# Kernel optimization log

Hardware: AMD Instinct MI355X
Metric: run time of the kernel (lower is better)

The kernel has to match this reference:

```python
import jax, jax.numpy as jnp
import numpy as np

N = 10000      # nodes
E = 100000     # edges
H = 256        # hidden_dim
HEADS = 4
HD = H // HEADS
G = 8          # graphs in batch
SPG = N // G   # nodes per graph (equal-size graphs -> to_dense_batch is a reshape)
IN = 16        # in_dim
PE = 5         # pe_dims
ED = 8         # edge_dim
OUT = 4        # out_dim
L = 5          # num_layers


def setup_inputs() -> dict:
    key = jax.random.key(0)
    ks = iter(jax.random.split(key, 64))
    rn = lambda shape, s=0.05: jax.random.normal(next(ks), shape, jnp.float32) * s
    inp = {}
    inp['x'] = jax.random.normal(next(ks), (N, IN), jnp.float32)
    inp['pe'] = jax.random.normal(next(ks), (N, PE), jnp.float32)
    inp['edge_attr'] = jax.random.normal(next(ks), (E, ED), jnp.float32)
    inp['edge_index'] = jax.random.randint(next(ks), (2, E), 0, N, jnp.int32)
    inp['batch'] = (jnp.arange(N) // SPG).astype(jnp.int32)
    # node encoders (3 node types), stacked
    inp['enc_w1'] = rn((3, IN + PE, H)); inp['enc_b1'] = rn((3, H))
    inp['enc_w2'] = rn((3, H, H));       inp['enc_b2'] = rn((3, H))
    # edge encoder
    inp['ee_w1'] = rn((ED, H)); inp['ee_b1'] = rn((H,))
    inp['ee_w2'] = rn((H, H));  inp['ee_b2'] = rn((H,))
    # per-layer edge / node update MLPs, stacked over layers
    inp['eu_w1'] = rn((L, 3 * H, H)); inp['eu_b1'] = rn((L, H))
    inp['eu_w2'] = rn((L, H, H));     inp['eu_b2'] = rn((L, H))
    inp['nu_w1'] = rn((L, 2 * H, H)); inp['nu_b1'] = rn((L, H))
    inp['nu_w2'] = rn((L, H, H));     inp['nu_b2'] = rn((L, H))
    # MultiheadAttention (combined in-proj + out-proj)
    inp['qkv_w'] = rn((H, 3 * H)); inp['qkv_b'] = rn((3 * H,))
    inp['out_w'] = rn((H, H));     inp['out_b'] = rn((H,))
    # fusion MLP
    inp['fu_w1'] = rn((H, H)); inp['fu_b1'] = rn((H,))
    inp['fu_w2'] = rn((H, H)); inp['fu_b2'] = rn((H,))
    # decoders (3 node types)
    inp['dec_w1'] = rn((3, H, H));   inp['dec_b1'] = rn((3, H))
    inp['dec_w2'] = rn((3, H, OUT)); inp['dec_b2'] = rn((3, OUT))
    return inp


def _mlp(z, w1, b1, w2, b2):
    return jnp.maximum(z @ w1 + b1, 0.0) @ w2 + b2


def reference(x, pe, edge_attr, edge_index, batch,
              enc_w1, enc_b1, enc_w2, enc_b2,
              ee_w1, ee_b1, ee_w2, ee_b2,
              eu_w1, eu_b1, eu_w2, eu_b2,
              nu_w1, nu_b1, nu_w2, nu_b2,
              qkv_w, qkv_b, out_w, out_b,
              fu_w1, fu_b1, fu_w2, fu_b2,
              dec_w1, dec_b1, dec_w2, dec_b2):
    n = x.shape[0]
    node_types = (jnp.clip(jnp.round(x[:, 2] * 3.0), 1.0, 3.0).astype(jnp.int32) - 1)
    rng_n = jnp.arange(n)

    # node encoding: run all 3 type-MLPs, select per node (masked dispatch in torch)
    inp = jnp.concatenate([x, pe], axis=-1)                       # [N, IN+PE]
    hid = jnp.maximum(jnp.einsum('ni,tih->tnh', inp, enc_w1) + enc_b1[:, None, :], 0.0)
    h_all = jnp.einsum('tnh,tho->tno', hid, enc_w2) + enc_b2[:, None, :]  # [3,N,H]
    h_nodes = h_all[node_types, rng_n]                            # [N, H]

    h_edges = _mlp(edge_attr, ee_w1, ee_b1, ee_w2, ee_b2)         # [E, H]

    src, dst = edge_index[0], edge_index[1]
    for l in range(L):
        e_in = jnp.concatenate([h_nodes[src], h_nodes[dst], h_edges], axis=-1)  # [E,3H]
        h_edges = h_edges + _mlp(e_in, eu_w1[l], eu_b1[l], eu_w2[l], eu_b2[l])
        m_node = jax.ops.segment_sum(h_edges, dst, num_segments=n)              # index_add_
        n_in = jnp.concatenate([h_nodes, m_node], axis=-1)                      # [N,2H]
        h_nodes = h_nodes + _mlp(n_in, nu_w1[l], nu_b1[l], nu_w2[l], nu_b2[l])

    # global attention: equal-size graphs -> to_dense_batch is a reshape, mask all-true
    xp = h_nodes.reshape(G, SPG, H)
    qkv = xp @ qkv_w + qkv_b                                      # [G,S,3H]
    q, k, v = jnp.split(qkv, 3, axis=-1)
    split_heads = lambda t: t.reshape(G, SPG, HEADS, HD).transpose(0, 2, 1, 3)
    q, k, v = split_heads(q), split_heads(k), split_heads(v)
    scale = 1.0 / np.sqrt(HD).astype(np.float32)
    att = jax.nn.softmax(jnp.einsum('ghsd,ghtd->ghst', q, k) * scale, axis=-1)
    o = jnp.einsum('ghst,ghtd->ghsd', att, v).transpose(0, 2, 1, 3).reshape(G, SPG, H)
    glob = (xp + (o @ out_w + out_b)).reshape(n, H)

    h = _mlp(h_nodes + glob, fu_w1, fu_b1, fu_w2, fu_b2)

    dhid = jnp.maximum(jnp.einsum('nh,tho->tno', h, dec_w1) + dec_b1[:, None, :], 0.0)
    out_all = jnp.einsum('tno,tok->tnk', dhid, dec_w2) + dec_b2[:, None, :]     # [3,N,OUT]
    return out_all[node_types, rng_n]
```

## Files before the change

### kernel.cpp

```cpp
#include <hip/hip_runtime.h>
#include <hip/hip_bf16.h>
#include <math.h>

#define NN 10000
#define NE 100000
#define SPGc 1250
#define NG 8
#define NL 5
#define ECHK 25000

__device__ __forceinline__ int imin(int a, int b) { return a < b ? a : b; }

__global__ __launch_bounds__(256) void k_types(const float* __restrict__ x, int* __restrict__ types) {
    int i = blockIdx.x * 256 + threadIdx.x;
    if (i < NN) {
        float v = rintf(x[(size_t)i * 16 + 2] * 3.0f);
        v = fminf(fmaxf(v, 1.0f), 3.0f);
        types[i] = (int)v - 1;
    }
}

__global__ __launch_bounds__(256) void k_hist(const int* __restrict__ dst, int* __restrict__ deg) {
    int e = blockIdx.x * 256 + threadIdx.x;
    if (e < NE) atomicAdd(&deg[dst[e]], 1);
}

__global__ __launch_bounds__(256) void k_scan(const int* __restrict__ deg, int* __restrict__ row_ptr,
                                              int* __restrict__ cursor) {
    __shared__ int buf[256];
    int tid = threadIdx.x;
    int base = 0;
    for (int c = 0; c < NN; c += 256) {
        int i = c + tid;
        int v = (i < NN) ? deg[i] : 0;
        buf[tid] = v;
        __syncthreads();
        for (int off = 1; off < 256; off <<= 1) {
            int t = (tid >= off) ? buf[tid - off] : 0;
            __syncthreads();
            buf[tid] += t;
            __syncthreads();
        }
        if (i < NN) {
            row_ptr[i + 1] = base + buf[tid];
            cursor[i] = base + buf[tid] - v;
        }
        __syncthreads();
        base += buf[255];
        __syncthreads();
    }
    if (tid == 0) row_ptr[0] = 0;
}

__global__ __launch_bounds__(256) void k_scatter(const int* __restrict__ dst, int* __restrict__ cursor,
                                                 int* __restrict__ csr) {
    int e = blockIdx.x * 256 + threadIdx.x;
    if (e < NE) {
        int p = atomicAdd(&cursor[dst[e]], 1);
        csr[p] = e;
    }
}

__global__ __launch_bounds__(256) void k_enc(const float* __restrict__ x, const float* __restrict__ pe,
        const int* __restrict__ types,
        const float* __restrict__ w1, const float* __restrict__ b1,
        const float* __restrict__ w2, const float* __restrict__ b2,
        float* __restrict__ h_nodes) {
    int n = blockIdx.x;
    int j = threadIdx.x;
    __shared__ float inp[21];
    __shared__ float hid[256];
    if (j < 16) inp[j] = x[(size_t)n * 16 + j];
    else if (j < 21) inp[j] = pe[(size_t)n * 5 + (j - 16)];
    __syncthreads();
    int t = types[n];
    const float* W1 = w1 + (size_t)t * 21 * 256;
    float a = b1[t * 256 + j];
    #pragma unroll
    for (int i = 0; i < 21; ++i) a = fmaf(inp[i], W1[i * 256 + j], a);
    hid[j] = fmaxf(a, 0.f);
    __syncthreads();
    const float* W2 = w2 + (size_t)t * 256 * 256;
    float o = b2[t * 256 + j];
    for (int k = 0; k < 256; ++k) o = fmaf(hid[k], W2[k * 256 + j], o);
    h_nodes[(size_t)n * 256 + j] = o;
}

__global__ __launch_bounds__(256) void gemm64(int Mrows, int K, int Nout,
        const float* __restrict__ A0, int lda,
        const float* __restrict__ W, const float* __restrict__ bias,
        float* __restrict__ C) {
    __shared__ __align__(16) float As[16][68];
    __shared__ __align__(16) float Ws[16][64];
    int tid = threadIdx.x;
    int tx = tid & 15, ty = tid >> 4;
    int blockRow = blockIdx.x * 64;
    int ncol0 = blockIdx.y * 64;
    float acc[4][4];
    #pragma unroll
    for (int i = 0; i < 4; ++i)
        #pragma unroll
        for (int j = 0; j < 4; ++j) acc[i][j] = 0.f;

    for (int k0 = 0; k0 < K; k0 += 16) {
        #pragma unroll
        for (int i = 0; i < 4; ++i) {
            int id = tid + 256 * i;
            int kk = id & 15, r = id >> 4;
            int grow = blockRow + r;
            int k = k0 + kk;
            float v = 0.f;
            if (grow < Mrows && k < K) v = A0[(size_t)grow * lda + k];
            As[kk][r] = v;
        }
        #pragma unroll
        for (int i = 0; i < 4; ++i) {
            int id = tid + 256 * i;
            int c = id & 63, kk = id >> 6;
            int k = k0 + kk;
            Ws[kk][c] = (k < K) ? W[(size_t)k * Nout + ncol0 + c] : 0.f;
        }
        __syncthreads();
        #pragma unroll
        for (int kk = 0; kk < 16; ++kk) {
            const float4 a4 = *(const float4*)&As[kk][ty << 2];
            const float4 w4 = *(const float4*)&Ws[kk][tx << 2];
            float av[4] = {a4.x, a4.y, a4.z, a4.w};
            float wv[4] = {w4.x, w4.y, w4.z, w4.w};
            #pragma unroll
            for (int i = 0; i < 4; ++i)
                #pragma unroll
                for (int j = 0; j < 4; ++j)
                    acc[i][j] = fmaf(av[i], wv[j], acc[i][j]);
        }
        __syncthreads();
    }
    #pragma unroll
    for (int i = 0; i < 4; ++i) {
        int grow = blockRow + (ty << 2) + i;
        if (grow >= Mrows) continue;
        size_t base = (size_t)grow * Nout + ncol0 + (tx << 2);
        #pragma unroll
        for (int j = 0; j < 4; ++j)
            C[base + j] = fmaxf(acc[i][j] + bias[ncol0 + (tx << 2) + j], 0.f);
    }
}

template<int AMODE, bool RELU, bool HASRES, bool PGATH, bool HASBIAS>
__global__ __launch_bounds__(256) void gemm_f32(int Mrows, int K, int Nout,
        const float* __restrict__ A0, const float* __restrict__ A1, int lda, int rowOfsA,
        const int* __restrict__ gsrc, const int* __restrict__ gdst,
        const float* __restrict__ Pa, const float* __restrict__ Pb,
        const float* __restrict__ W, const float* __restrict__ bias,
        const float* __restrict__ ResF, float resScale, int rowOfsC,
        float* __restrict__ C) {
    __shared__ __align__(16) float As[16][68];
    __shared__ __align__(16) float Ws[16][16][20];
    int tid = threadIdx.x;
    int blockRow = blockIdx.x * 64;
    int ncol0 = blockIdx.y * 256;
    int r4 = tid >> 4, c16 = tid & 15;
    int sar = tid >> 2, sak = (tid & 3) * 4;
    int swk = tid >> 4, scg = tid & 15;
    float acc[4][16];
    #pragma unroll
    for (int i = 0; i < 4; ++i)
        #pragma unroll
        for (int n = 0; n < 16; ++n) acc[i][n] = 0.f;

    for (int k0 = 0; k0 < K; k0 += 16) {
        {
            int arow = imin(blockRow + sar, Mrows - 1) + rowOfsA;
            float4 av;
            if (AMODE == 0) {
                av = *(const float4*)(A0 + (size_t)arow * lda + k0 + sak);
            } else {
                int k = k0 + sak;
                av = (k < 256) ? *(const float4*)(A0 + (size_t)arow * 256 + k)
                               : *(const float4*)(A1 + (size_t)arow * 256 + (k - 256));
            }
            As[sak + 0][sar] = av.x;
            As[sak + 1][sar] = av.y;
            As[sak + 2][sar] = av.z;
            As[sak + 3][sar] = av.w;
        }
        {
            const float* wp = W + (size_t)(k0 + swk) * Nout + ncol0 + scg * 16;
            *(float4*)&Ws[swk][scg][0]  = *(const float4*)(wp + 0);
            *(float4*)&Ws[swk][scg][4]  = *(const float4*)(wp + 4);
            *(float4*)&Ws[swk][scg][8]  = *(const float4*)(wp + 8);
            *(float4*)&Ws[swk][scg][12] = *(const float4*)(wp + 12);
        }
        __syncthreads();
        #pragma unroll
        for (int kk = 0; kk < 16; ++kk) {
            const float4 a4 = *(const float4*)&As[kk][r4 << 2];
            float av[4] = {a4.x, a4.y, a4.z, a4.w};
            #pragma unroll
            for (int q = 0; q < 4; ++q) {
                const float4 w4 = *(const float4*)&Ws[kk][c16][q << 2];
                float wv[4] = {w4.x, w4.y, w4.z, w4.w};
                #pragma unroll
                for (int i = 0; i < 4; ++i)
                    #pragma unroll
                    for (int j = 0; j < 4; ++j)
                        acc[i][q * 4 + j] = fmaf(av[i], wv[j], acc[i][q * 4 + j]);
            }
        }
        __syncthreads();
    }
    #pragma unroll
    for (int i = 0; i < 4; ++i) {
        int grow = blockRow + (r4 << 2) + i;
        if (grow >= Mrows) continue;
        size_t crow = (size_t)(grow + rowOfsC);
        int colb = ncol0 + (c16 << 4);
        const float* par = nullptr;
        const float* pbr = nullptr;
        if (PGATH) {
            int e = grow + rowOfsA;
            par = Pa + (size_t)gsrc[e] * 256 + colb;
            pbr = Pb + (size_t)gdst[e] * 256 + colb;
        }
        #pragma unroll
        for (int q = 0; q < 4; ++q) {
            float v[4];
            #pragma unroll
            for (int j = 0; j < 4; ++j) v[j] = acc[i][q * 4 + j];
            if (HASBIAS) {
                const float4 b4 = *(const float4*)(bias + colb + q * 4);
                v[0] += b4.x; v[1] += b4.y; v[2] += b4.z; v[3] += b4.w;
            }
            if (PGATH) {
                const float4 pa4 = *(const float4*)(par + q * 4);
                const float4 pb4 = *(const float4*)(pbr + q * 4);
                v[0] += pa4.x + pb4.x; v[1] += pa4.y + pb4.y;
                v[2] += pa4.z + pb4.z; v[3] += pa4.w + pb4.w;
            }
            if (RELU) {
                v[0] = fmaxf(v[0], 0.f); v[1] = fmaxf(v[1], 0.f);
                v[2] = fmaxf(v[2], 0.f); v[3] = fmaxf(v[3], 0.f);
            }
            if (HASRES) {
                const float4 rv = *(const float4*)(ResF + crow * Nout + colb + q * 4);
                v[0] += resScale * rv.x; v[1] += resScale * rv.y;
                v[2] += resScale * rv.z; v[3] += resScale * rv.w;
            }
            float4 o; o.x = v[0]; o.y = v[1]; o.z = v[2]; o.w = v[3];
            *(float4*)(C + crow * Nout + colb + q * 4) = o;
        }
    }
}

__global__ __launch_bounds__(256) void k_mnode(const float* __restrict__ h_edges,
        const int* __restrict__ row_ptr, const int* __restrict__ csr, float* __restrict__ m_node) {
    int n = blockIdx.x * 4 + (threadIdx.x >> 6);
    int lane = threadIdx.x & 63;
    if (n >= NN) return;
    float a0 = 0.f, a1 = 0.f, a2 = 0.f, a3 = 0.f;
    int s = row_ptr[n], e = row_ptr[n + 1];
    for (int i = s; i < e; ++i) {
        int ed = csr[i];
        const float4 v = *(const float4*)(h_edges + (size_t)ed * 256 + (lane << 2));
        a0 += v.x; a1 += v.y; a2 += v.z; a3 += v.w;
    }
    float4 r; r.x = a0; r.y = a1; r.z = a2; r.w = a3;
    *(float4*)(m_node + (size_t)n * 256 + (lane << 2)) = r;
}

__global__ __launch_bounds__(256) void k_attn(const float* __restrict__ qkv, float* __restrict__ obuf) {
    int gh = blockIdx.y;
    int g = gh >> 2, h = gh & 3;
    int q0 = blockIdx.x * 64;
    int tid = threadIdx.x;
    int r = tid >> 2, q4 = tid & 3;
    int d0 = q4 * 16;
    __shared__ __align__(16) float Ks[32][64];
    __shared__ __align__(16) float Vs[32][64];
    const float* base = qkv + (size_t)g * SPGc * 768;
    int my_s = q0 + r;
    bool rowok = my_s < SPGc;
    float qreg[16];
    #pragma unroll
    for (int dd = 0; dd < 16; ++dd) qreg[dd] = 0.f;
    if (rowok) {
        const float* qp = base + (size_t)my_s * 768 + h * 64 + d0;
        #pragma unroll
        for (int dd = 0; dd < 16; ++dd) qreg[dd] = qp[dd];
    }
    float m = -1e30f, l = 0.f;
    float oacc[16];
    #pragma unroll
    for (int dd = 0; dd < 16; ++dd) oacc[dd] = 0.f;

    for (int t0 = 0; t0 < SPGc; t0 += 32) {
        #pragma unroll
        for (int i = 0; i < 8; ++i) {
            int id = tid + 256 * i;
            int d = id & 63, jj = id >> 6;
            int s = t0 + jj;
            float kv = 0.f, vv = 0.f;
            if (s < SPGc) {
                const float* kp = base + (size_t)s * 768 + h * 64;
                kv = kp[256 + d];
                vv = kp[512 + d];
            }
            Ks[jj][d] = kv;
            Vs[jj][d] = vv;
        }
        __syncthreads();
        float sc[32];
        #pragma unroll
        for (int j = 0; j < 32; ++j) {
            float p = 0.f;
            #pragma unroll
            for (int dd = 0; dd < 16; dd += 4) {
                const float4 k4 = *(const float4*)&Ks[j][d0 + dd];
                p = fmaf(qreg[dd], k4.x, p);
                p = fmaf(qreg[dd + 1], k4.y, p);
                p = fmaf(qreg[dd + 2], k4.z, p);
                p = fmaf(qreg[dd + 3], k4.w, p);
            }
            sc[j] = p;
        }
        #pragma unroll
        for (int j = 0; j < 32; ++j) {
            float p = sc[j];
            p += __shfl_xor(p, 1);
            p += __shfl_xor(p, 2);
            sc[j] = (t0 + j < SPGc) ? p * 0.125f : -1e30f;
        }
        float mt = sc[0];
        #pragma unroll
        for (int j = 1; j < 32; ++j) mt = fmaxf(mt, sc[j]);
        float mnew = fmaxf(m, mt);
        float f = __expf(m - mnew);
        l *= f;
        #pragma unroll
        for (int dd = 0; dd < 16; ++dd) oacc[dd] *= f;
        #pragma unroll
        for (int j = 0; j < 32; ++j) {
            float p = __expf(sc[j] - mnew);
            l += p;
            #pragma unroll
            for (int dd = 0; dd < 16; dd += 4) {
                const float4 v4 = *(const float4*)&Vs[j][d0 + dd];
                oacc[dd]     = fmaf(p, v4.x, oacc[dd]);
                oacc[dd + 1] = fmaf(p, v4.y, oacc[dd + 1]);
                oacc[dd + 2] = fmaf(p, v4.z, oacc[dd + 2]);
                oacc[dd + 3] = fmaf(p, v4.w, oacc[dd + 3]);
            }
        }
        m = mnew;
        __syncthreads();
    }
    if (rowok) {
        float rinv = 1.0f / l;
        float* op = obuf + (size_t)(g * SPGc + my_s) * 256 + h * 64 + d0;
        #pragma unroll
        for (int dd = 0; dd < 16; ++dd) op[dd] = oacc[dd] * rinv;
    }
}

__global__ __launch_bounds__(256) void k_dec(const float* __restrict__ h, const int* __restrict__ types,
        const float* __restrict__ w1, const float* __restrict__ b1,
        const float* __restrict__ w2, const float* __restrict__ b2,
        float* __restrict__ out) {
    int n = blockIdx.x;
    int j = threadIdx.x;
    __shared__ float hrow[256];
    __shared__ float dhid[256];
    hrow[j] = h[(size_t)n * 256 + j];
    __syncthreads();
    int t = types[n];
    const float* W1 = w1 + (size_t)t * 256 * 256;
    float a = b1[t * 256 + j];
    for (int k = 0; k < 256; ++k) a = fmaf(hrow[k], W1[k * 256 + j], a);
    dhid[j] = fmaxf(a, 0.f);
    __syncthreads();
    int lane = j & 63, w = j >> 6;
    const float* W2 = w2 + (size_t)t * 256 * 4;
    float p = 0.f;
    #pragma unroll
    for (int q = 0; q < 4; ++q) {
        int kk = lane + 64 * q;
        p = fmaf(dhid[kk], W2[kk * 4 + w], p);
    }
    #pragma unroll
    for (int o2 = 32; o2 > 0; o2 >>= 1) p += __shfl_down(p, o2);
    if (lane == 0) out[(size_t)n * 4 + w] = p + b2[t * 4 + w];
}

extern "C" void kernel_launch(void* const* d_in, const int* in_sizes, int n_in,
                              void* d_out, int out_size, void* d_ws, size_t ws_size,
                              hipStream_t stream) {
    const float* x         = (const float*)d_in[0];
    const float* pe        = (const float*)d_in[1];
    const float* edge_attr = (const float*)d_in[2];
    const int*   eidx      = (const int*)d_in[3];
    const float* enc_w1 = (const float*)d_in[5];
    const float* enc_b1 = (const float*)d_in[6];
    const float* enc_w2 = (const float*)d_in[7];
    const float* enc_b2 = (const float*)d_in[8];
    const float* ee_w1  = (const float*)d_in[9];
    const float* ee_b1  = (const float*)d_in[10];
    const float* ee_w2  = (const float*)d_in[11];
    const float* ee_b2  = (const float*)d_in[12];
    const float* eu_w1  = (const float*)d_in[13];
    const float* eu_b1  = (const float*)d_in[14];
    const float* eu_w2  = (const float*)d_in[15];
    const float* eu_b2  = (const float*)d_in[16];
    const float* nu_w1  = (const float*)d_in[17];
    const float* nu_b1  = (const float*)d_in[18];
    const float* nu_w2  = (const float*)d_in[19];
    const float* nu_b2  = (const float*)d_in[20];
    const float* qkv_w  = (const float*)d_in[21];
    const float* qkv_b  = (const float*)d_in[22];
    const float* out_w  = (const float*)d_in[23];
    const float* out_b  = (const float*)d_in[24];
    const float* fu_w1  = (const float*)d_in[25];
    const float* fu_b1  = (const float*)d_in[26];
    const float* fu_w2  = (const float*)d_in[27];
    const float* fu_b2  = (const float*)d_in[28];
    const float* dec_w1 = (const float*)d_in[29];
    const float* dec_b1 = (const float*)d_in[30];
    const float* dec_w2 = (const float*)d_in[31];
    const float* dec_b2 = (const float*)d_in[32];

    const int* src  = eidx;
    const int* dstp = eidx + NE;

    float* ws = (float*)d_ws;
    float* h_edges = ws;
    float* big     = ws + 25600000;
    float* h_nodes = ws + 37120000;
    float* mn_ob   = ws + 39680000;
    float* nhid    = ws + 42240000;
    int* ibase   = (int*)(ws + 44800000);
    int* types   = ibase;
    int* deg     = ibase + NN;
    int* row_ptr = deg + NN;
    int* cursor  = row_ptr + NN + 1;
    int* csr     = cursor + NN;

    float* ehid = big;
    float* Pa   = big + 6400000;
    float* Pb   = big + 8960000;
    float* qkvf = big;
    float* fin  = big + 7680000;

    hipMemsetAsync(deg, 0, NN * sizeof(int), stream);
    k_types<<<(NN + 255) / 256, 256, 0, stream>>>(x, types);
    k_hist<<<(NE + 255) / 256, 256, 0, stream>>>(dstp, deg);
    k_scan<<<1, 256, 0, stream>>>(deg, row_ptr, cursor);
    k_scatter<<<(NE + 255) / 256, 256, 0, stream>>>(dstp, cursor, csr);

    k_enc<<<NN, 256, 0, stream>>>(x, pe, types, enc_w1, enc_b1, enc_w2, enc_b2, h_nodes);

    dim3 gE((ECHK + 63) / 64, 1);
    dim3 gN((NN + 63) / 64, 1);

    for (int c0 = 0; c0 < NE; c0 += ECHK) {
        gemm64<<<dim3((ECHK + 63) / 64, 4), 256, 0, stream>>>(ECHK, 8, 256,
            edge_attr + (size_t)c0 * 8, 8, ee_w1, ee_b1, ehid);
        gemm_f32<0, false, false, false, true><<<gE, 256, 0, stream>>>(ECHK, 256, 256,
            ehid, nullptr, 256, 0, nullptr, nullptr, nullptr, nullptr,
            ee_w2, ee_b2, nullptr, 0.f, c0, h_edges);
    }

    for (int l = 0; l < NL; ++l) {
        const float* W1 = eu_w1 + (size_t)l * 768 * 256;
        gemm_f32<0, false, false, false, false><<<gN, 256, 0, stream>>>(NN, 256, 256,
            h_nodes, nullptr, 256, 0, nullptr, nullptr, nullptr, nullptr,
            W1, nullptr, nullptr, 0.f, 0, Pa);
        gemm_f32<0, false, false, false, false><<<gN, 256, 0, stream>>>(NN, 256, 256,
            h_nodes, nullptr, 256, 0, nullptr, nullptr, nullptr, nullptr,
            W1 + 65536, nullptr, nullptr, 0.f, 0, Pb);
        for (int c0 = 0; c0 < NE; c0 += ECHK) {
            gemm_f32<0, true, false, true, true><<<gE, 256, 0, stream>>>(ECHK, 256, 256,
                h_edges, nullptr, 256, c0, src, dstp, Pa, Pb,
                W1 + 131072, eu_b1 + l * 256, nullptr, 0.f, 0, ehid);
            gemm_f32<0, false, true, false, true><<<gE, 256, 0, stream>>>(ECHK, 256, 256,
                ehid, nullptr, 256, 0, nullptr, nullptr, nullptr, nullptr,
                eu_w2 + (size_t)l * 65536, eu_b2 + l * 256, h_edges, 1.f, c0, h_edges);
        }
        k_mnode<<<(NN + 3) / 4, 256, 0, stream>>>(h_edges, row_ptr, csr, mn_ob);
        gemm_f32<2, true, false, false, true><<<gN, 256, 0, stream>>>(NN, 512, 256,
            h_nodes, mn_ob, 256, 0, nullptr, nullptr, nullptr, nullptr,
            nu_w1 + (size_t)l * 131072, nu_b1 + l * 256, nullptr, 0.f, 0, nhid);
        gemm_f32<0, false, true, false, true><<<gN, 256, 0, stream>>>(NN, 256, 256,
            nhid, nullptr, 256, 0, nullptr, nullptr, nullptr, nullptr,
            nu_w2 + (size_t)l * 65536, nu_b2 + l * 256, h_nodes, 1.f, 0, h_nodes);
    }

    gemm_f32<0, false, false, false, true><<<dim3((NN + 63) / 64, 3), 256, 0, stream>>>(NN, 256, 768,
        h_nodes, nullptr, 256, 0, nullptr, nullptr, nullptr, nullptr,
        qkv_w, qkv_b, nullptr, 0.f, 0, qkvf);

    dim3 ga((SPGc + 63) / 64, NG * 4);
    k_attn<<<ga, 256, 0, stream>>>(qkvf, mn_ob);

    gemm_f32<0, false, true, false, true><<<gN, 256, 0, stream>>>(NN, 256, 256,
        mn_ob, nullptr, 256, 0, nullptr, nullptr, nullptr, nullptr,
        out_w, out_b, h_nodes, 2.f, 0, fin);
    gemm_f32<0, true, false, false, true><<<gN, 256, 0, stream>>>(NN, 256, 256,
        fin, nullptr, 256, 0, nullptr, nullptr, nullptr, nullptr,
        fu_w1, fu_b1, nullptr, 0.f, 0, nhid);
    gemm_f32<0, false, false, false, true><<<gN, 256, 0, stream>>>(NN, 256, 256,
        nhid, nullptr, 256, 0, nullptr, nullptr, nullptr, nullptr,
        fu_w2, fu_b2, nullptr, 0.f, 0, mn_ob);

    k_dec<<<NN, 256, 0, stream>>>(mn_ob, types, dec_w1, dec_b1, dec_w2, dec_b2, (float*)d_out);
}
```

Measured before the change: 4.436 ms.

## Halve GEMM column tile, split attention keys across blocks, unroll encoder/decoder loops

The FP32 GEMM tile narrows from 64x256 to 64x128 output columns per block, so twice as many blocks launch and each thread holds fewer accumulators. Attention is split over four key partitions (flash-decoding style) and a new merge kernel combines the per-partition max, sum and outputs, reusing the h_edges buffer as scratch. The encoder and decoder inner loops get an unroll-by-8 pragma. The aim is better occupancy and CU fill, at the cost of reloading the A tile twice per row block and an extra kernel with a partial-result round trip through memory.

After: 4.200 ms. 5.3% less time.

```diff
diff --git a/kernel.cpp b/kernel.cpp
--- a/kernel.cpp
+++ b/kernel.cpp
@@ -8,6 +8,7 @@
 #define NG 8
 #define NL 5
 #define ECHK 25000
+#define NROWS_A (NG * 4 * SPGc)
 
 __device__ __forceinline__ int imin(int a, int b) { return a < b ? a : b; }
 
@@ -82,6 +83,7 @@
     __syncthreads();
     const float* W2 = w2 + (size_t)t * 256 * 256;
     float o = b2[t * 256 + j];
+    #pragma unroll 8
     for (int k = 0; k < 256; ++k) o = fmaf(hid[k], W2[k * 256 + j], o);
     h_nodes[(size_t)n * 256 + j] = o;
 }
@@ -155,18 +157,18 @@
         const float* __restrict__ ResF, float resScale, int rowOfsC,
         float* __restrict__ C) {
     __shared__ __align__(16) float As[16][68];
-    __shared__ __align__(16) float Ws[16][16][20];
+    __shared__ __align__(16) float Ws[16][16][10];
     int tid = threadIdx.x;
     int blockRow = blockIdx.x * 64;
-    int ncol0 = blockIdx.y * 256;
-    int r4 = tid >> 4, c16 = tid & 15;
+    int ncol0 = blockIdx.y * 128;
+    int rg = tid >> 4, cg = tid & 15;
     int sar = tid >> 2, sak = (tid & 3) * 4;
     int swk = tid >> 4, scg = tid & 15;
-    float acc[4][16];
+    float acc[4][8];
     #pragma unroll
     for (int i = 0; i < 4; ++i)
         #pragma unroll
-        for (int n = 0; n < 16; ++n) acc[i][n] = 0.f;
+        for (int n = 0; n < 8; ++n) acc[i][n] = 0.f;
 
     for (int k0 = 0; k0 < K; k0 += 16) {
         {
@@ -185,36 +187,32 @@
             As[sak + 3][sar] = av.w;
         }
         {
-            const float* wp = W + (size_t)(k0 + swk) * Nout + ncol0 + scg * 16;
-            *(float4*)&Ws[swk][scg][0]  = *(const float4*)(wp + 0);
-            *(float4*)&Ws[swk][scg][4]  = *(const float4*)(wp + 4);
-            *(float4*)&Ws[swk][scg][8]  = *(const float4*)(wp + 8);
-            *(float4*)&Ws[swk][scg][12] = *(const float4*)(wp + 12);
+            const float* wp = W + (size_t)(k0 + swk) * Nout + ncol0 + scg * 8;
+            *(float4*)&Ws[swk][scg][0] = *(const float4*)(wp + 0);
+            *(float4*)&Ws[swk][scg][4] = *(const float4*)(wp + 4);
         }
         __syncthreads();
         #pragma unroll
         for (int kk = 0; kk < 16; ++kk) {
-            const float4 a4 = *(const float4*)&As[kk][r4 << 2];
+            const float4 a4 = *(const float4*)&As[kk][rg << 2];
             float av[4] = {a4.x, a4.y, a4.z, a4.w};
+            const float4 w0 = *(const float4*)&Ws[kk][cg][0];
+            const float4 w1 = *(const float4*)&Ws[kk][cg][4];
+            float wv[8] = {w0.x, w0.y, w0.z, w0.w, w1.x, w1.y, w1.z, w1.w};
             #pragma unroll
-            for (int q = 0; q < 4; ++q) {
-                const float4 w4 = *(const float4*)&Ws[kk][c16][q << 2];
-                float wv[4] = {w4.x, w4.y, w4.z, w4.w};
+            for (int i = 0; i < 4; ++i)
                 #pragma unroll
-                for (int i = 0; i < 4; ++i)
-                    #pragma unroll
-                    for (int j = 0; j < 4; ++j)
-                        acc[i][q * 4 + j] = fmaf(av[i], wv[j], acc[i][q * 4 + j]);
-            }
+                for (int j = 0; j < 8; ++j)
+                    acc[i][j] = fmaf(av[i], wv[j], acc[i][j]);
         }
         __syncthreads();
     }
     #pragma unroll
     for (int i = 0; i < 4; ++i) {
-        int grow = blockRow + (r4 << 2) + i;
+        int grow = blockRow + (rg << 2) + i;
         if (grow >= Mrows) continue;
         size_t crow = (size_t)(grow + rowOfsC);
-        int colb = ncol0 + (c16 << 4);
+        int colb = ncol0 + (cg << 3);
         const float* par = nullptr;
         const float* pbr = nullptr;
         if (PGATH) {
@@ -223,7 +221,7 @@
             pbr = Pb + (size_t)gdst[e] * 256 + colb;
         }
         #pragma unroll
-        for (int q = 0; q < 4; ++q) {
+        for (int q = 0; q < 2; ++q) {
             float v[4];
             #pragma unroll
             for (int j = 0; j < 4; ++j) v[j] = acc[i][q * 4 + j];
@@ -268,9 +266,14 @@
     *(float4*)(m_node + (size_t)n * 256 + (lane << 2)) = r;
 }
 
-__global__ __launch_bounds__(256) void k_attn(const float* __restrict__ qkv, float* __restrict__ obuf) {
-    int gh = blockIdx.y;
+__global__ __launch_bounds__(256) void k_attn_part(const float* __restrict__ qkv,
+        float* __restrict__ opart, float* __restrict__ mpart, float* __restrict__ lpart) {
+    int y = blockIdx.y;
+    int p = y & 3;
+    int gh = y >> 2;
     int g = gh >> 2, h = gh & 3;
+    int kb = p * 313;
+    int ke = imin(kb + 313, SPGc);
     int q0 = blockIdx.x * 64;
     int tid = threadIdx.x;
     int r = tid >> 2, q4 = tid & 3;
@@ -293,14 +296,14 @@
     #pragma unroll
     for (int dd = 0; dd < 16; ++dd) oacc[dd] = 0.f;
 
-    for (int t0 = 0; t0 < SPGc; t0 += 32) {
+    for (int t0 = kb; t0 < ke; t0 += 32) {
         #pragma unroll
         for (int i = 0; i < 8; ++i) {
             int id = tid + 256 * i;
             int d = id & 63, jj = id >> 6;
             int s = t0 + jj;
             float kv = 0.f, vv = 0.f;
-            if (s < SPGc) {
+            if (s < ke) {
                 const float* kp = base + (size_t)s * 768 + h * 64;
                 kv = kp[256 + d];
                 vv = kp[512 + d];
@@ -312,23 +315,23 @@
         float sc[32];
         #pragma unroll
         for (int j = 0; j < 32; ++j) {
-            float p = 0.f;
+            float pq = 0.f;
             #pragma unroll
             for (int dd = 0; dd < 16; dd += 4) {
                 const float4 k4 = *(const float4*)&Ks[j][d0 + dd];
-                p = fmaf(qreg[dd], k4.x, p);
-                p = fmaf(qreg[dd + 1], k4.y, p);
-                p = fmaf(qreg[dd + 2], k4.z, p);
-                p = fmaf(qreg[dd + 3], k4.w, p);
-            }
-            sc[j] = p;
+                pq = fmaf(qreg[dd], k4.x, pq);
+                pq = fmaf(qreg[dd + 1], k4.y, pq);
+                pq = fmaf(qreg[dd + 2], k4.z, pq);
+                pq = fmaf(qreg[dd + 3], k4.w, pq);
+            }
+            sc[j] = pq;
         }
         #pragma unroll
         for (int j = 0; j < 32; ++j) {
-            float p = sc[j];
-            p += __shfl_xor(p, 1);
-            p += __shfl_xor(p, 2);
-            sc[j] = (t0 + j < SPGc) ? p * 0.125f : -1e30f;
+            float pq = sc[j];
+            pq += __shfl_xor(pq, 1);
+            pq += __shfl_xor(pq, 2);
+            sc[j] = (t0 + j < ke) ? pq * 0.125f : -1e30f;
         }
         float mt = sc[0];
         #pragma unroll
@@ -340,26 +343,50 @@
         for (int dd = 0; dd < 16; ++dd) oacc[dd] *= f;
         #pragma unroll
         for (int j = 0; j < 32; ++j) {
-            float p = __expf(sc[j] - mnew);
-            l += p;
+            float pq = __expf(sc[j] - mnew);
+            l += pq;
             #pragma unroll
             for (int dd = 0; dd < 16; dd += 4) {
                 const float4 v4 = *(const float4*)&Vs[j][d0 + dd];
-                oacc[dd]     = fmaf(p, v4.x, oacc[dd]);
-                oacc[dd + 1] = fmaf(p, v4.y, oacc[dd + 1]);
-                oacc[dd + 2] = fmaf(p, v4.z, oacc[dd + 2]);
-                oacc[dd + 3] = fmaf(p, v4.w, oacc[dd + 3]);
+                oacc[dd]     = fmaf(pq, v4.x, oacc[dd]);
+                oacc[dd + 1] = fmaf(pq, v4.y, oacc[dd + 1]);
+                oacc[dd + 2] = fmaf(pq, v4.z, oacc[dd + 2]);
+                oacc[dd + 3] = fmaf(pq, v4.w, oacc[dd + 3]);
             }
         }
         m = mnew;
         __syncthreads();
     }
     if (rowok) {
-        float rinv = 1.0f / l;
-        float* op = obuf + (size_t)(g * SPGc + my_s) * 256 + h * 64 + d0;
-        #pragma unroll
-        for (int dd = 0; dd < 16; ++dd) op[dd] = oacc[dd] * rinv;
-    }
+        size_t R = (size_t)gh * SPGc + my_s;
+        float* op = opart + (R * 4 + p) * 64 + d0;
+        #pragma unroll
+        for (int dd = 0; dd < 16; ++dd) op[dd] = oacc[dd];
+        if (q4 == 0) {
+            mpart[R * 4 + p] = m;
+            lpart[R * 4 + p] = l;
+        }
+    }
+}
+
+__global__ __launch_bounds__(256) void k_amerge(const float* __restrict__ opart,
+        const float* __restrict__ mpart, const float* __restrict__ lpart,
+        float* __restrict__ obuf) {
+    int R = blockIdx.x * 4 + (threadIdx.x >> 6);
+    int lane = threadIdx.x & 63;
+    if (R >= NROWS_A) return;
+    float m0 = mpart[R * 4 + 0], m1 = mpart[R * 4 + 1];
+    float m2 = mpart[R * 4 + 2], m3 = mpart[R * 4 + 3];
+    float ms = fmaxf(fmaxf(m0, m1), fmaxf(m2, m3));
+    float w0 = __expf(m0 - ms), w1 = __expf(m1 - ms);
+    float w2 = __expf(m2 - ms), w3 = __expf(m3 - ms);
+    float l = w0 * lpart[R * 4 + 0] + w1 * lpart[R * 4 + 1]
+            + w2 * lpart[R * 4 + 2] + w3 * lpart[R * 4 + 3];
+    const float* ob = opart + (size_t)R * 4 * 64 + lane;
+    float o = w0 * ob[0] + w1 * ob[64] + w2 * ob[128] + w3 * ob[192];
+    int gh = R / SPGc, s = R % SPGc;
+    int g = gh >> 2, h = gh & 3;
+    obuf[((size_t)(g * SPGc + s)) * 256 + h * 64 + lane] = o / l;
 }
 
 __global__ __launch_bounds__(256) void k_dec(const float* __restrict__ h, const int* __restrict__ types,
@@ -375,6 +402,7 @@
     int t = types[n];
     const float* W1 = w1 + (size_t)t * 256 * 256;
     float a = b1[t * 256 + j];
+    #pragma unroll 8
     for (int k = 0; k < 256; ++k) a = fmaf(hrow[k], W1[k * 256 + j], a);
     dhid[j] = fmaxf(a, 0.f);
     __syncthreads();
@@ -449,6 +477,10 @@
     float* qkvf = big;
     float* fin  = big + 7680000;
 
+    float* opart = h_edges;
+    float* mpart = h_edges + 10240000;
+    float* lpart = h_edges + 10400000;
+
     hipMemsetAsync(deg, 0, NN * sizeof(int), stream);
     k_types<<<(NN + 255) / 256, 256, 0, stream>>>(x, types);
     k_hist<<<(NE + 255) / 256, 256, 0, stream>>>(dstp, deg);
@@ -457,8 +489,8 @@
 
     k_enc<<<NN, 256, 0, stream>>>(x, pe, types, enc_w1, enc_b1, enc_w2, enc_b2, h_nodes);
 
-    dim3 gE((ECHK + 63) / 64, 1);
-    dim3 gN((NN + 63) / 64, 1);
+    dim3 gE((ECHK + 63) / 64, 2);
+    dim3 gN((NN + 63) / 64, 2);
 
     for (int c0 = 0; c0 < NE; c0 += ECHK) {
         gemm64<<<dim3((ECHK + 63) / 64, 4), 256, 0, stream>>>(ECHK, 8, 256,
@@ -493,12 +525,13 @@
             nu_w2 + (size_t)l * 65536, nu_b2 + l * 256, h_nodes, 1.f, 0, h_nodes);
     }
 
-    gemm_f32<0, false, false, false, true><<<dim3((NN + 63) / 64, 3), 256, 0, stream>>>(NN, 256, 768,
+    gemm_f32<0, false, false, false, true><<<dim3((NN + 63) / 64, 6), 256, 0, stream>>>(NN, 256, 768,
         h_nodes, nullptr, 256, 0, nullptr, nullptr, nullptr, nullptr,
         qkv_w, qkv_b, nullptr, 0.f, 0, qkvf);
 
-    dim3 ga((SPGc + 63) / 64, NG * 4);
-    k_attn<<<ga, 256, 0, stream>>>(qkvf, mn_ob);
+    dim3 ga((SPGc + 63) / 64, NG * 4 * 4);
+    k_attn_part<<<ga, 256, 0, stream>>>(qkvf, opart, mpart, lpart);
+    k_amerge<<<(NROWS_A + 3) / 4, 256, 0, stream>>>(opart, mpart, lpart, mn_ob);
 
     gemm_f32<0, false, true, false, true><<<gN, 256, 0, stream>>>(NN, 256, 256,
         mn_ob, nullptr, 256, 0, nullptr, nullptr, nullptr, nullptr,
```
